# Performance work log

Hardware: AMD Instinct MI355X
Metric: run time of the kernel (lower is better)

Reference implementation:

```python
import jax, jax.numpy as jnp
import numpy as np

E, H, HD = 2048, 32, 64
SCALE = HD ** -0.5


def setup_inputs() -> dict:
    key = jax.random.key(0)
    ks = jax.random.split(key, 11)
    B, T, P = 16, 4, 4096
    S = P + T
    return {
        "hidden_states": jax.random.normal(ks[0], (B, T, E), jnp.float32),
        "past_key": jax.random.normal(ks[1], (1, H, P, HD), jnp.float32),
        "past_value": jax.random.normal(ks[2], (1, H, P, HD), jnp.float32),
        "attention_mask": jnp.zeros((B, 1, T, S), jnp.float32),
        "Wq": jax.random.normal(ks[3], (E, E), jnp.float32) * 0.02,
        "bq": jax.random.normal(ks[4], (E,), jnp.float32) * 0.02,
        "Wk": jax.random.normal(ks[5], (E, E), jnp.float32) * 0.02,
        "bk": jax.random.normal(ks[6], (E,), jnp.float32) * 0.02,
        "Wv": jax.random.normal(ks[7], (E, E), jnp.float32) * 0.02,
        "bv": jax.random.normal(ks[8], (E,), jnp.float32) * 0.02,
        "Wo": jax.random.normal(ks[9], (E, E), jnp.float32) * 0.02,
        "bo": jax.random.normal(ks[10], (E,), jnp.float32) * 0.02,
    }


def _shape(x, B, S):
    # [B,S,E] -> [B,H,S,hd]
    return x.reshape(B, S, H, HD).transpose(0, 2, 1, 3)


def reference(hidden_states, past_key, past_value, attention_mask,
              Wq, bq, Wk, bk, Wv, bv, Wo, bo):
    B, T, _ = hidden_states.shape
    # projections (torch Linear: x @ W.T + b); query pre-scaled
    q = _shape(hidden_states @ Wq.T + bq, B, T) * SCALE   # [B,H,T,hd]
    k_new = _shape(hidden_states @ Wk.T + bk, B, T)       # [B,H,T,hd]
    v_new = _shape(hidden_states @ Wv.T + bv, B, T)
    # cache stored with batch 1, broadcast (torch repeat) to B, then concat
    k_past = jnp.broadcast_to(past_key, (B,) + past_key.shape[1:])
    v_past = jnp.broadcast_to(past_value, (B,) + past_value.shape[1:])
    k = jnp.concatenate([k_past, k_new], axis=2)          # [B,H,S,hd]
    v = jnp.concatenate([v_past, v_new], axis=2)
    scores = jnp.einsum('bhtd,bhsd->bhts', q, k)          # [B,H,T,S]
    scores = scores + attention_mask                      # mask is [B,1,T,S]
    scores = jnp.maximum(scores, jnp.finfo(scores.dtype).min)
    w = jax.nn.softmax(scores, axis=-1)
    out = jnp.einsum('bhts,bhsd->bhtd', w, v)             # [B,H,T,hd]
    out = out.transpose(0, 2, 1, 3).reshape(B, T, E)
    return out @ Wo.T + bo
```

## Files before the change

kernel.cpp:

```cpp
#include <hip/hip_runtime.h>
#include <hip/hip_bf16.h>


typedef float f4 __attribute__((ext_vector_type(4)));
typedef short s8v __attribute__((ext_vector_type(8)));

#define NEG_HUGE (-3.402823466e38f)

__device__ inline unsigned short f2bs(float x) {
  union { float f; unsigned int u; } a; a.f = x;
  unsigned int u = a.u;
  u += 0x7fffu + ((u >> 16) & 1u);
  return (unsigned short)(u >> 16);
}
__device__ inline float bs2f(unsigned short s) {
  union { unsigned int u; float f; } a; a.u = ((unsigned int)s) << 16;
  return a.f;
}
__device__ inline unsigned int pk2(float a, float b) {
  union { __hip_bfloat162 v; unsigned int u; } c;
  c.v = __float22bfloat162_rn(make_float2(a, b));
  return c.u;
}
__device__ inline unsigned long long pack4(float a, float b, float c, float d) {
  return (unsigned long long)pk2(a, b) | ((unsigned long long)pk2(c, d) << 32);
}
__device__ inline s8v cvt8(f4 a, f4 b) {
  union { s8v s; unsigned int u[4]; } r;
  r.u[0] = pk2(a[0], a[1]); r.u[1] = pk2(a[2], a[3]);
  r.u[2] = pk2(b[0], b[1]); r.u[3] = pk2(b[2], b[3]);
  return r.s;
}
__device__ inline f4 mfma16(s8v a, s8v b, f4 c) {
  return __builtin_amdgcn_mfma_f32_16x16x32_bf16(a, b, c, 0, 0, 0);
}
__device__ inline f4 fzero() { f4 z = {0.f,0.f,0.f,0.f}; return z; }
__device__ inline float wave_sum(float v) {
  #pragma unroll
  for (int off = 32; off; off >>= 1) v += __shfl_xor(v, off, 64);
  return v;
}

__global__ __launch_bounds__(256) void k_qkv(
    const float* __restrict__ hs, const float* __restrict__ Wq,
    const float* __restrict__ Wk, const float* __restrict__ Wv,
    float* __restrict__ part) {
  __shared__ __align__(16) unsigned short As[64 * 264];
  const int n0 = blockIdx.x * 64;
  const int k0 = blockIdx.y * 256;
  const int p = n0 >> 11;
  const int c0 = n0 & 2047;
  const float* W = (p == 0) ? Wq : (p == 1) ? Wk : Wv;
  const int t = threadIdx.x, lane = t & 63, w = t >> 6;
  const int cl = lane & 15, quad = lane >> 4;

  #pragma unroll
  for (int i = 0; i < 16; ++i) {
    int idx4 = t + (i << 8);
    int row = idx4 >> 6;
    int col = (idx4 & 63) << 2;
    f4 v = *reinterpret_cast<const f4*>(hs + row * 2048 + k0 + col);
    *reinterpret_cast<unsigned long long*>(&As[row * 264 + col]) =
        pack4(v[0], v[1], v[2], v[3]);
  }
  __syncthreads();

  f4 acc[4];
  #pragma unroll
  for (int i = 0; i < 4; ++i) acc[i] = fzero();

  const int cw = c0 + w * 16 + cl;
  const float* wbase = W + (size_t)cw * 2048 + k0;
  #pragma unroll
  for (int ks2 = 0; ks2 < 8; ++ks2) {
    const int kb = ks2 * 32 + quad * 8;
    f4 w0 = *reinterpret_cast<const f4*>(wbase + kb);
    f4 w1 = *reinterpret_cast<const f4*>(wbase + kb + 4);
    s8v bf = cvt8(w0, w1);
    #pragma unroll
    for (int mt = 0; mt < 4; ++mt) {
      s8v af = *reinterpret_cast<const s8v*>(&As[(mt * 16 + cl) * 264 + kb]);
      acc[mt] = mfma16(af, bf, acc[mt]);
    }
  }
  float* outp = part + (size_t)blockIdx.y * 64 * 6144;
  #pragma unroll
  for (int mt = 0; mt < 4; ++mt)
    #pragma unroll
    for (int rg = 0; rg < 4; ++rg) {
      int r = mt * 16 + quad * 4 + rg;
      outp[r * 6144 + n0 + w * 16 + cl] = acc[mt][rg];
    }
}

__global__ __launch_bounds__(256) void k_qkv_red(
    const float* __restrict__ part, const float* __restrict__ bq,
    const float* __restrict__ bk, const float* __restrict__ bv,
    unsigned short* __restrict__ qws, float* __restrict__ knew,
    float* __restrict__ vnew) {
  const int i4 = blockIdx.x * 256 + threadIdx.x;
  const int base = i4 * 4;
  const int r = base / 6144;
  const int n = base - r * 6144;
  f4 s = *reinterpret_cast<const f4*>(part + base);
  #pragma unroll
  for (int ks = 1; ks < 8; ++ks) {
    f4 p2 = *reinterpret_cast<const f4*>(part + (size_t)ks * 393216 + base);
    #pragma unroll
    for (int j = 0; j < 4; ++j) s[j] += p2[j];
  }
  const int p = n >> 11, c = n & 2047;
  const int h = c >> 6, d = c & 63;
  const int b = r >> 2, tt = r & 3;
  if (p == 0) {
    f4 bb = *reinterpret_cast<const f4*>(bq + c);
    uint2 pw;
    pw.x = pk2((s[0] + bb[0]) * 0.125f, (s[1] + bb[1]) * 0.125f);
    pw.y = pk2((s[2] + bb[2]) * 0.125f, (s[3] + bb[3]) * 0.125f);
    *reinterpret_cast<uint2*>(qws + h * 4608 + r * 72 + d) = pw;
  } else if (p == 1) {
    f4 bb = *reinterpret_cast<const f4*>(bk + c);
    f4 o;
    #pragma unroll
    for (int j = 0; j < 4; ++j) o[j] = s[j] + bb[j];
    *reinterpret_cast<f4*>(knew + ((h * 16 + b) * 4 + tt) * 64 + d) = o;
  } else {
    f4 bb = *reinterpret_cast<const f4*>(bv + c);
    f4 o;
    #pragma unroll
    for (int j = 0; j < 4; ++j) o[j] = s[j] + bb[j];
    *reinterpret_cast<f4*>(vnew + ((h * 16 + b) * 4 + tt) * 64 + d) = o;
  }
}

__global__ __launch_bounds__(256) void k_flash(
    const unsigned short* __restrict__ qws, const float* __restrict__ Kp,
    const float* __restrict__ Vp, const float* __restrict__ mask,
    float* __restrict__ Opart, float* __restrict__ mpart,
    float* __restrict__ lpart) {
  __shared__ __align__(16) unsigned short Pl[64 * 264];
  __shared__ float redm[4 * 64];
  __shared__ float reds[4 * 64];
  const int bx = blockIdx.x;
  const int h = bx & 31, cch = bx >> 5;
  const int s0 = cch * 256;
  const int t = threadIdx.x, lane = t & 63, w = t >> 6;
  const int cl = lane & 15, quad = lane >> 4;
  const float* Kh = Kp + (size_t)h * 4096 * 64;
  const float* Vh = Vp + (size_t)h * 4096 * 64;

  s8v qf[4][2];
  #pragma unroll
  for (int qt = 0; qt < 4; ++qt)
    #pragma unroll
    for (int k2 = 0; k2 < 2; ++k2)
      qf[qt][k2] = *reinterpret_cast<const s8v*>(
          qws + h * 4608 + (qt * 16 + cl) * 72 + k2 * 32 + quad * 8);

  f4 acc[4][4];
  #pragma unroll
  for (int si = 0; si < 4; ++si)
    #pragma unroll
    for (int qt = 0; qt < 4; ++qt)
      acc[si][qt] = *reinterpret_cast<const f4*>(
          mask + (size_t)(qt * 16 + cl) * 4100 + s0 + w * 64 + si * 16 + quad * 4);

  f4 kreg[4][2][2];
  #pragma unroll
  for (int si = 0; si < 4; ++si) {
    const float* kr = Kh + (size_t)(s0 + w * 64 + si * 16 + cl) * 64 + quad * 8;
    #pragma unroll
    for (int k2 = 0; k2 < 2; ++k2) {
      kreg[si][k2][0] = *reinterpret_cast<const f4*>(kr + k2 * 32);
      kreg[si][k2][1] = *reinterpret_cast<const f4*>(kr + k2 * 32 + 4);
    }
  }

  #pragma unroll
  for (int si = 0; si < 4; ++si)
    #pragma unroll
    for (int k2 = 0; k2 < 2; ++k2) {
      s8v ak = cvt8(kreg[si][k2][0], kreg[si][k2][1]);
      #pragma unroll
      for (int qt = 0; qt < 4; ++qt)
        acc[si][qt] = mfma16(ak, qf[qt][k2], acc[si][qt]);
    }

  #pragma unroll
  for (int si = 0; si < 4; ++si)
    #pragma unroll
    for (int qt = 0; qt < 4; ++qt)
      #pragma unroll
      for (int rg = 0; rg < 4; ++rg)
        acc[si][qt][rg] = fmaxf(acc[si][qt][rg], NEG_HUGE);

  #pragma unroll
  for (int qt = 0; qt < 4; ++qt) {
    float m = NEG_HUGE;
    #pragma unroll
    for (int si = 0; si < 4; ++si)
      #pragma unroll
      for (int rg = 0; rg < 4; ++rg) m = fmaxf(m, acc[si][qt][rg]);
    m = fmaxf(m, __shfl_xor(m, 16, 64));
    m = fmaxf(m, __shfl_xor(m, 32, 64));
    if (quad == 0) redm[w * 64 + qt * 16 + cl] = m;
  }
  __syncthreads();

  const int dcol = w * 16 + cl;
  float vr[8][8];
  #pragma unroll
  for (int k2 = 0; k2 < 8; ++k2) {
    const int sb = k2 * 32 + quad * 8;
    const float* vb = Vh + (size_t)(s0 + sb) * 64 + dcol;
    #pragma unroll
    for (int j = 0; j < 8; ++j) vr[k2][j] = vb[j * 64];
  }

  float mq[4];
  #pragma unroll
  for (int qt = 0; qt < 4; ++qt) {
    int q = qt * 16 + cl;
    mq[qt] = fmaxf(fmaxf(redm[q], redm[64 + q]),
                   fmaxf(redm[128 + q], redm[192 + q]));
    if (w == 0 && quad == 0) mpart[(h * 16 + cch) * 64 + q] = mq[qt];
  }
  #pragma unroll
  for (int qt = 0; qt < 4; ++qt) {
    float sum = 0.f;
    #pragma unroll
    for (int si = 0; si < 4; ++si) {
      f4 e;
      #pragma unroll
      for (int rg = 0; rg < 4; ++rg) {
        e[rg] = __expf(acc[si][qt][rg] - mq[qt]);
        sum += e[rg];
      }
      uint2 pw;
      pw.x = pk2(e[0], e[1]);
      pw.y = pk2(e[2], e[3]);
      *reinterpret_cast<uint2*>(
          &Pl[(qt * 16 + cl) * 264 + w * 64 + si * 16 + quad * 4]) = pw;
    }
    sum += __shfl_xor(sum, 16, 64);
    sum += __shfl_xor(sum, 32, 64);
    if (quad == 0) reds[w * 64 + qt * 16 + cl] = sum;
  }
  __syncthreads();

  if (w == 0 && quad == 0) {
    #pragma unroll
    for (int qt = 0; qt < 4; ++qt) {
      int q = qt * 16 + cl;
      lpart[(h * 16 + cch) * 64 + q] =
          reds[q] + reds[64 + q] + reds[128 + q] + reds[192 + q];
    }
  }

  f4 oacc[4];
  #pragma unroll
  for (int mt = 0; mt < 4; ++mt) oacc[mt] = fzero();
  #pragma unroll
  for (int k2 = 0; k2 < 8; ++k2) {
    const int sb = k2 * 32 + quad * 8;
    f4 v0, v1;
    v0[0] = vr[k2][0]; v0[1] = vr[k2][1]; v0[2] = vr[k2][2]; v0[3] = vr[k2][3];
    v1[0] = vr[k2][4]; v1[1] = vr[k2][5]; v1[2] = vr[k2][6]; v1[3] = vr[k2][7];
    s8v bvv = cvt8(v0, v1);
    #pragma unroll
    for (int mt = 0; mt < 4; ++mt) {
      s8v pa = *reinterpret_cast<const s8v*>(&Pl[(mt * 16 + cl) * 264 + sb]);
      oacc[mt] = mfma16(pa, bvv, oacc[mt]);
    }
  }
  float* ob = Opart + (size_t)(h * 16 + cch) * 64 * 64;
  #pragma unroll
  for (int mt = 0; mt < 4; ++mt)
    #pragma unroll
    for (int rg = 0; rg < 4; ++rg)
      ob[(mt * 16 + quad * 4 + rg) * 64 + dcol] = oacc[mt][rg];
}

__global__ __launch_bounds__(256) void k_merge(
    const unsigned short* __restrict__ qws, const float* __restrict__ knew,
    const float* __restrict__ vnew, const float* __restrict__ mask,
    const float* __restrict__ Opart, const float* __restrict__ mpart,
    const float* __restrict__ lpart, unsigned short* __restrict__ attn) {
  const int bx = blockIdx.x;
  const int h = bx & 31, b = bx >> 5;
  const int tt = threadIdx.x >> 6;
  const int d = threadIdx.x & 63;
  const int r = b * 4 + tt;
  float qd = bs2f(qws[h * 4608 + r * 72 + d]);
  float scn[4];
  #pragma unroll
  for (int tp = 0; tp < 4; ++tp) {
    float kn = knew[((h * 16 + b) * 4 + tp) * 64 + d];
    float s = wave_sum(qd * kn);
    s += mask[(size_t)r * 4100 + 4096 + tp];
    scn[tp] = fmaxf(s, NEG_HUGE);
  }
  float mi[16], li[16];
  float mtot = NEG_HUGE;
  #pragma unroll
  for (int i = 0; i < 16; ++i) {
    mi[i] = mpart[(h * 16 + i) * 64 + r];
    li[i] = lpart[(h * 16 + i) * 64 + r];
    mtot = fmaxf(mtot, mi[i]);
  }
  #pragma unroll
  for (int tp = 0; tp < 4; ++tp) mtot = fmaxf(mtot, scn[tp]);
  float ltot = 0.f, od = 0.f;
  #pragma unroll
  for (int i = 0; i < 16; ++i) {
    float fct = __expf(mi[i] - mtot);
    ltot += li[i] * fct;
    od += Opart[((size_t)(h * 16 + i) * 64 + r) * 64 + d] * fct;
  }
  #pragma unroll
  for (int tp = 0; tp < 4; ++tp) {
    float e = __expf(scn[tp] - mtot);
    ltot += e;
    od += e * vnew[((h * 16 + b) * 4 + tp) * 64 + d];
  }
  attn[(size_t)r * 2048 + h * 64 + d] = f2bs(od / ltot);
}

__global__ __launch_bounds__(256) void k_out(
    const unsigned short* __restrict__ attn, const float* __restrict__ Wo,
    float* __restrict__ part) {
  __shared__ __align__(16) unsigned short As[64 * 264];
  const int n0 = blockIdx.x * 64;
  const int ksb = blockIdx.y;
  const int k0 = ksb * 256;
  const int t = threadIdx.x, lane = t & 63, w = t >> 6;
  const int cl = lane & 15, quad = lane >> 4;
  #pragma unroll
  for (int i = 0; i < 8; ++i) {
    int idx8 = t + (i << 8);
    int row = idx8 >> 5;
    int col = (idx8 & 31) << 3;
    *reinterpret_cast<uint4*>(&As[row * 264 + col]) =
        *reinterpret_cast<const uint4*>(attn + (size_t)row * 2048 + k0 + col);
  }
  __syncthreads();
  f4 acc[4];
  #pragma unroll
  for (int i = 0; i < 4; ++i) acc[i] = fzero();
  const int cw = n0 + w * 16 + cl;
  const float* wbase = Wo + (size_t)cw * 2048 + k0;
  #pragma unroll
  for (int ks2 = 0; ks2 < 8; ++ks2) {
    const int kb = ks2 * 32 + quad * 8;
    f4 w0 = *reinterpret_cast<const f4*>(wbase + kb);
    f4 w1 = *reinterpret_cast<const f4*>(wbase + kb + 4);
    s8v bf = cvt8(w0, w1);
    #pragma unroll
    for (int mt = 0; mt < 4; ++mt) {
      s8v af = *reinterpret_cast<const s8v*>(&As[(mt * 16 + cl) * 264 + kb]);
      acc[mt] = mfma16(af, bf, acc[mt]);
    }
  }
  float* op = part + (size_t)ksb * 131072;
  #pragma unroll
  for (int mt = 0; mt < 4; ++mt)
    #pragma unroll
    for (int rg = 0; rg < 4; ++rg) {
      int r = mt * 16 + quad * 4 + rg;
      op[r * 2048 + n0 + w * 16 + cl] = acc[mt][rg];
    }
}

__global__ __launch_bounds__(256) void k_out_red(
    const float* __restrict__ part, const float* __restrict__ bo,
    float* __restrict__ out) {
  const int i4 = blockIdx.x * 256 + threadIdx.x;
  f4 s = *reinterpret_cast<const f4*>(part + (size_t)i4 * 4);
  #pragma unroll
  for (int ks = 1; ks < 8; ++ks) {
    f4 p2 = *reinterpret_cast<const f4*>(part + (size_t)ks * 131072 + (size_t)i4 * 4);
    #pragma unroll
    for (int j = 0; j < 4; ++j) s[j] += p2[j];
  }
  f4 bias = *reinterpret_cast<const f4*>(bo + (i4 & 511) * 4);
  f4 o;
  #pragma unroll
  for (int j = 0; j < 4; ++j) o[j] = s[j] + bias[j];
  *reinterpret_cast<f4*>(out + (size_t)i4 * 4) = o;
}

extern "C" void kernel_launch(void* const* d_in, const int* in_sizes, int n_in,
                              void* d_out, int out_size, void* d_ws, size_t ws_size,
                              hipStream_t stream) {
  const float* hs   = (const float*)d_in[0];
  const float* pk   = (const float*)d_in[1];
  const float* pv   = (const float*)d_in[2];
  const float* mask = (const float*)d_in[3];
  const float* Wq   = (const float*)d_in[4];
  const float* bq   = (const float*)d_in[5];
  const float* Wk   = (const float*)d_in[6];
  const float* bk   = (const float*)d_in[7];
  const float* Wv   = (const float*)d_in[8];
  const float* bv   = (const float*)d_in[9];
  const float* Wo   = (const float*)d_in[10];
  const float* bo   = (const float*)d_in[11];

  float* f = (float*)d_ws;
  float* qkv_part = f;
  float* o_part   = qkv_part + 3145728;
  float* Opart    = o_part   + 1048576;
  float* mpart    = Opart    + 2097152;
  float* lpart    = mpart    + 32768;
  float* knew     = lpart    + 32768;
  float* vnew     = knew     + 131072;
  unsigned short* qws  = (unsigned short*)(vnew + 131072);
  unsigned short* attn = qws + 147456;

  k_qkv<<<dim3(96, 8), 256, 0, stream>>>(hs, Wq, Wk, Wv, qkv_part);
  k_qkv_red<<<384, 256, 0, stream>>>(qkv_part, bq, bk, bv, qws, knew, vnew);
  k_flash<<<512, 256, 0, stream>>>(qws, pk, pv, mask, Opart, mpart, lpart);
  k_merge<<<512, 256, 0, stream>>>(qws, knew, vnew, mask, Opart, mpart, lpart, attn);
  k_out<<<dim3(32, 8), 256, 0, stream>>>(attn, Wo, o_part);
  k_out_red<<<128, 256, 0, stream>>>(o_part, bo, (float*)d_out);
}
```

Before: 197.4 us.

## Fuse QKV split-K reduction into flash and merge kernels, drop reduce launch

Removes the separate k_qkv_red kernel. Each flash block now sums the eight split-K partials for its head's Q slice, adds the bias, scales and stores the result as bf16 in shared memory. The merge kernel sums the partials for its own q, k_new and v_new directly. This saves one kernel launch and the intermediate qws/knew/vnew buffers, but the Q reduction is repeated across the 16 chunk blocks per head, and merge reads the partials with scalar loads.

```diff
diff --git a/kernel.cpp b/kernel.cpp
--- a/kernel.cpp
+++ b/kernel.cpp
@@ -93,52 +93,13 @@
     }
 }
 
-__global__ __launch_bounds__(256) void k_qkv_red(
+__global__ __launch_bounds__(256) void k_flash(
     const float* __restrict__ part, const float* __restrict__ bq,
-    const float* __restrict__ bk, const float* __restrict__ bv,
-    unsigned short* __restrict__ qws, float* __restrict__ knew,
-    float* __restrict__ vnew) {
-  const int i4 = blockIdx.x * 256 + threadIdx.x;
-  const int base = i4 * 4;
-  const int r = base / 6144;
-  const int n = base - r * 6144;
-  f4 s = *reinterpret_cast<const f4*>(part + base);
-  #pragma unroll
-  for (int ks = 1; ks < 8; ++ks) {
-    f4 p2 = *reinterpret_cast<const f4*>(part + (size_t)ks * 393216 + base);
-    #pragma unroll
-    for (int j = 0; j < 4; ++j) s[j] += p2[j];
-  }
-  const int p = n >> 11, c = n & 2047;
-  const int h = c >> 6, d = c & 63;
-  const int b = r >> 2, tt = r & 3;
-  if (p == 0) {
-    f4 bb = *reinterpret_cast<const f4*>(bq + c);
-    uint2 pw;
-    pw.x = pk2((s[0] + bb[0]) * 0.125f, (s[1] + bb[1]) * 0.125f);
-    pw.y = pk2((s[2] + bb[2]) * 0.125f, (s[3] + bb[3]) * 0.125f);
-    *reinterpret_cast<uint2*>(qws + h * 4608 + r * 72 + d) = pw;
-  } else if (p == 1) {
-    f4 bb = *reinterpret_cast<const f4*>(bk + c);
-    f4 o;
-    #pragma unroll
-    for (int j = 0; j < 4; ++j) o[j] = s[j] + bb[j];
-    *reinterpret_cast<f4*>(knew + ((h * 16 + b) * 4 + tt) * 64 + d) = o;
-  } else {
-    f4 bb = *reinterpret_cast<const f4*>(bv + c);
-    f4 o;
-    #pragma unroll
-    for (int j = 0; j < 4; ++j) o[j] = s[j] + bb[j];
-    *reinterpret_cast<f4*>(vnew + ((h * 16 + b) * 4 + tt) * 64 + d) = o;
-  }
-}
-
-__global__ __launch_bounds__(256) void k_flash(
-    const unsigned short* __restrict__ qws, const float* __restrict__ Kp,
-    const float* __restrict__ Vp, const float* __restrict__ mask,
-    float* __restrict__ Opart, float* __restrict__ mpart,
-    float* __restrict__ lpart) {
+    const float* __restrict__ Kp, const float* __restrict__ Vp,
+    const float* __restrict__ mask, float* __restrict__ Opart,
+    float* __restrict__ mpart, float* __restrict__ lpart) {
   __shared__ __align__(16) unsigned short Pl[64 * 264];
+  __shared__ __align__(16) unsigned short Qs[64 * 72];
   __shared__ float redm[4 * 64];
   __shared__ float reds[4 * 64];
   const int bx = blockIdx.x;
@@ -149,13 +110,37 @@
   const float* Kh = Kp + (size_t)h * 4096 * 64;
   const float* Vh = Vp + (size_t)h * 4096 * 64;
 
+  {
+    const int hbase = h * 64;
+    #pragma unroll
+    for (int i = 0; i < 4; ++i) {
+      const int u = t + i * 256;
+      const int row = u >> 4;
+      const int c4 = (u & 15) << 2;
+      const int base = row * 6144 + hbase + c4;
+      f4 s = *reinterpret_cast<const f4*>(part + base);
+      #pragma unroll
+      for (int ks = 1; ks < 8; ++ks) {
+        f4 p2 = *reinterpret_cast<const f4*>(part + (size_t)ks * 393216 + base);
+        #pragma unroll
+        for (int j = 0; j < 4; ++j) s[j] += p2[j];
+      }
+      f4 bb = *reinterpret_cast<const f4*>(bq + hbase + c4);
+      uint2 pw;
+      pw.x = pk2((s[0] + bb[0]) * 0.125f, (s[1] + bb[1]) * 0.125f);
+      pw.y = pk2((s[2] + bb[2]) * 0.125f, (s[3] + bb[3]) * 0.125f);
+      *reinterpret_cast<uint2*>(&Qs[row * 72 + c4]) = pw;
+    }
+  }
+  __syncthreads();
+
   s8v qf[4][2];
   #pragma unroll
   for (int qt = 0; qt < 4; ++qt)
     #pragma unroll
     for (int k2 = 0; k2 < 2; ++k2)
       qf[qt][k2] = *reinterpret_cast<const s8v*>(
-          qws + h * 4608 + (qt * 16 + cl) * 72 + k2 * 32 + quad * 8);
+          &Qs[(qt * 16 + cl) * 72 + k2 * 32 + quad * 8]);
 
   f4 acc[4][4];
   #pragma unroll
@@ -282,21 +267,44 @@
 }
 
 __global__ __launch_bounds__(256) void k_merge(
-    const unsigned short* __restrict__ qws, const float* __restrict__ knew,
-    const float* __restrict__ vnew, const float* __restrict__ mask,
-    const float* __restrict__ Opart, const float* __restrict__ mpart,
-    const float* __restrict__ lpart, unsigned short* __restrict__ attn) {
+    const float* __restrict__ part, const float* __restrict__ bq,
+    const float* __restrict__ bk, const float* __restrict__ bv,
+    const float* __restrict__ mask, const float* __restrict__ Opart,
+    const float* __restrict__ mpart, const float* __restrict__ lpart,
+    unsigned short* __restrict__ attn) {
   const int bx = blockIdx.x;
   const int h = bx & 31, b = bx >> 5;
   const int tt = threadIdx.x >> 6;
   const int d = threadIdx.x & 63;
   const int r = b * 4 + tt;
-  float qd = bs2f(qws[h * 4608 + r * 72 + d]);
+  const int hbase = h * 64;
+
+  float qd;
+  {
+    float s = 0.f;
+    #pragma unroll
+    for (int ks = 0; ks < 8; ++ks)
+      s += part[(size_t)ks * 393216 + r * 6144 + hbase + d];
+    qd = (s + bq[hbase + d]) * 0.125f;
+  }
+  float kn[4], vn[4];
+  #pragma unroll
+  for (int tp = 0; tp < 4; ++tp) {
+    const int rr = b * 4 + tp;
+    float sk = 0.f, sv = 0.f;
+    #pragma unroll
+    for (int ks = 0; ks < 8; ++ks) {
+      sk += part[(size_t)ks * 393216 + rr * 6144 + 2048 + hbase + d];
+      sv += part[(size_t)ks * 393216 + rr * 6144 + 4096 + hbase + d];
+    }
+    kn[tp] = sk + bk[hbase + d];
+    vn[tp] = sv + bv[hbase + d];
+  }
+
   float scn[4];
   #pragma unroll
   for (int tp = 0; tp < 4; ++tp) {
-    float kn = knew[((h * 16 + b) * 4 + tp) * 64 + d];
-    float s = wave_sum(qd * kn);
+    float s = wave_sum(qd * kn[tp]);
     s += mask[(size_t)r * 4100 + 4096 + tp];
     scn[tp] = fmaxf(s, NEG_HUGE);
   }
@@ -321,7 +329,7 @@
   for (int tp = 0; tp < 4; ++tp) {
     float e = __expf(scn[tp] - mtot);
     ltot += e;
-    od += e * vnew[((h * 16 + b) * 4 + tp) * 64 + d];
+    od += e * vn[tp];
   }
   attn[(size_t)r * 2048 + h * 64 + d] = f2bs(od / ltot);
 }
@@ -411,15 +419,12 @@
   float* Opart    = o_part   + 1048576;
   float* mpart    = Opart    + 2097152;
   float* lpart    = mpart    + 32768;
-  float* knew     = lpart    + 32768;
-  float* vnew     = knew     + 131072;
-  unsigned short* qws  = (unsigned short*)(vnew + 131072);
-  unsigned short* attn = qws + 147456;
+  unsigned short* attn = (unsigned short*)(lpart + 32768);
 
   k_qkv<<<dim3(96, 8), 256, 0, stream>>>(hs, Wq, Wk, Wv, qkv_part);
-  k_qkv_red<<<384, 256, 0, stream>>>(qkv_part, bq, bk, bv, qws, knew, vnew);
-  k_flash<<<512, 256, 0, stream>>>(qws, pk, pv, mask, Opart, mpart, lpart);
-  k_merge<<<512, 256, 0, stream>>>(qws, knew, vnew, mask, Opart, mpart, lpart, attn);
+  k_flash<<<512, 256, 0, stream>>>(qkv_part, bq, pk, pv, mask, Opart, mpart, lpart);
+  k_merge<<<512, 256, 0, stream>>>(qkv_part, bq, bk, bv, mask, Opart, mpart,
+                                   lpart, attn);
   k_out<<<dim3(32, 8), 256, 0, stream>>>(attn, Wo, o_part);
   k_out_red<<<128, 256, 0, stream>>>(o_part, bo, (float*)d_out);
 }
```

Result: no change. 197.9 us (+0.2%).

## Double flash-decode block to 512 threads, splitting keys and PV reduction across waves

Applied to the files above, without the earlier changes.

The flash kernel now runs 8 waves per block instead of 4. Each wave covers 32 keys for QK^T and softmax. For the PV product, each wave handles one D tile over half of the key range, and writes a separate partial O slab. The merge kernel sums the two halves. This spreads the per-block K/V loading and MFMA work over more waves to raise memory-level parallelism and latency hiding. The cost is a doubled Opart workspace, extra merge reads, and more LDS reduction entries.

```diff
diff --git a/kernel.cpp b/kernel.cpp
--- a/kernel.cpp
+++ b/kernel.cpp
@@ -133,14 +133,14 @@
   }
 }
 
-__global__ __launch_bounds__(256) void k_flash(
+__global__ __launch_bounds__(512) void k_flash(
     const unsigned short* __restrict__ qws, const float* __restrict__ Kp,
     const float* __restrict__ Vp, const float* __restrict__ mask,
     float* __restrict__ Opart, float* __restrict__ mpart,
     float* __restrict__ lpart) {
   __shared__ __align__(16) unsigned short Pl[64 * 264];
-  __shared__ float redm[4 * 64];
-  __shared__ float reds[4 * 64];
+  __shared__ float redm[8 * 64];
+  __shared__ float reds[8 * 64];
   const int bx = blockIdx.x;
   const int h = bx & 31, cch = bx >> 5;
   const int s0 = cch * 256;
@@ -157,18 +157,18 @@
       qf[qt][k2] = *reinterpret_cast<const s8v*>(
           qws + h * 4608 + (qt * 16 + cl) * 72 + k2 * 32 + quad * 8);
 
-  f4 acc[4][4];
-  #pragma unroll
-  for (int si = 0; si < 4; ++si)
+  f4 acc[2][4];
+  #pragma unroll
+  for (int si = 0; si < 2; ++si)
     #pragma unroll
     for (int qt = 0; qt < 4; ++qt)
       acc[si][qt] = *reinterpret_cast<const f4*>(
-          mask + (size_t)(qt * 16 + cl) * 4100 + s0 + w * 64 + si * 16 + quad * 4);
-
-  f4 kreg[4][2][2];
-  #pragma unroll
-  for (int si = 0; si < 4; ++si) {
-    const float* kr = Kh + (size_t)(s0 + w * 64 + si * 16 + cl) * 64 + quad * 8;
+          mask + (size_t)(qt * 16 + cl) * 4100 + s0 + w * 32 + si * 16 + quad * 4);
+
+  f4 kreg[2][2][2];
+  #pragma unroll
+  for (int si = 0; si < 2; ++si) {
+    const float* kr = Kh + (size_t)(s0 + w * 32 + si * 16 + cl) * 64 + quad * 8;
     #pragma unroll
     for (int k2 = 0; k2 < 2; ++k2) {
       kreg[si][k2][0] = *reinterpret_cast<const f4*>(kr + k2 * 32);
@@ -177,7 +177,7 @@
   }
 
   #pragma unroll
-  for (int si = 0; si < 4; ++si)
+  for (int si = 0; si < 2; ++si)
     #pragma unroll
     for (int k2 = 0; k2 < 2; ++k2) {
       s8v ak = cvt8(kreg[si][k2][0], kreg[si][k2][1]);
@@ -187,7 +187,7 @@
     }
 
   #pragma unroll
-  for (int si = 0; si < 4; ++si)
+  for (int si = 0; si < 2; ++si)
     #pragma unroll
     for (int qt = 0; qt < 4; ++qt)
       #pragma unroll
@@ -198,7 +198,7 @@
   for (int qt = 0; qt < 4; ++qt) {
     float m = NEG_HUGE;
     #pragma unroll
-    for (int si = 0; si < 4; ++si)
+    for (int si = 0; si < 2; ++si)
       #pragma unroll
       for (int rg = 0; rg < 4; ++rg) m = fmaxf(m, acc[si][qt][rg]);
     m = fmaxf(m, __shfl_xor(m, 16, 64));
@@ -207,29 +207,32 @@
   }
   __syncthreads();
 
-  const int dcol = w * 16 + cl;
-  float vr[8][8];
-  #pragma unroll
-  for (int k2 = 0; k2 < 8; ++k2) {
-    const int sb = k2 * 32 + quad * 8;
+  const int dtile = w & 3, khalf = w >> 2;
+  const int dcol = dtile * 16 + cl;
+  float vr[4][8];
+  #pragma unroll
+  for (int k2l = 0; k2l < 4; ++k2l) {
+    const int sb = (khalf * 4 + k2l) * 32 + quad * 8;
     const float* vb = Vh + (size_t)(s0 + sb) * 64 + dcol;
     #pragma unroll
-    for (int j = 0; j < 8; ++j) vr[k2][j] = vb[j * 64];
+    for (int j = 0; j < 8; ++j) vr[k2l][j] = vb[j * 64];
   }
 
   float mq[4];
   #pragma unroll
   for (int qt = 0; qt < 4; ++qt) {
     int q = qt * 16 + cl;
-    mq[qt] = fmaxf(fmaxf(redm[q], redm[64 + q]),
-                   fmaxf(redm[128 + q], redm[192 + q]));
-    if (w == 0 && quad == 0) mpart[(h * 16 + cch) * 64 + q] = mq[qt];
+    float m = redm[q];
+    #pragma unroll
+    for (int ww = 1; ww < 8; ++ww) m = fmaxf(m, redm[ww * 64 + q]);
+    mq[qt] = m;
+    if (w == 0 && quad == 0) mpart[(h * 16 + cch) * 64 + q] = m;
   }
   #pragma unroll
   for (int qt = 0; qt < 4; ++qt) {
     float sum = 0.f;
     #pragma unroll
-    for (int si = 0; si < 4; ++si) {
+    for (int si = 0; si < 2; ++si) {
       f4 e;
       #pragma unroll
       for (int rg = 0; rg < 4; ++rg) {
@@ -240,7 +243,7 @@
       pw.x = pk2(e[0], e[1]);
       pw.y = pk2(e[2], e[3]);
       *reinterpret_cast<uint2*>(
-          &Pl[(qt * 16 + cl) * 264 + w * 64 + si * 16 + quad * 4]) = pw;
+          &Pl[(qt * 16 + cl) * 264 + w * 32 + si * 16 + quad * 4]) = pw;
     }
     sum += __shfl_xor(sum, 16, 64);
     sum += __shfl_xor(sum, 32, 64);
@@ -252,8 +255,10 @@
     #pragma unroll
     for (int qt = 0; qt < 4; ++qt) {
       int q = qt * 16 + cl;
-      lpart[(h * 16 + cch) * 64 + q] =
-          reds[q] + reds[64 + q] + reds[128 + q] + reds[192 + q];
+      float s = reds[q];
+      #pragma unroll
+      for (int ww = 1; ww < 8; ++ww) s += reds[ww * 64 + q];
+      lpart[(h * 16 + cch) * 64 + q] = s;
     }
   }
 
@@ -261,11 +266,11 @@
   #pragma unroll
   for (int mt = 0; mt < 4; ++mt) oacc[mt] = fzero();
   #pragma unroll
-  for (int k2 = 0; k2 < 8; ++k2) {
-    const int sb = k2 * 32 + quad * 8;
+  for (int k2l = 0; k2l < 4; ++k2l) {
+    const int sb = (khalf * 4 + k2l) * 32 + quad * 8;
     f4 v0, v1;
-    v0[0] = vr[k2][0]; v0[1] = vr[k2][1]; v0[2] = vr[k2][2]; v0[3] = vr[k2][3];
-    v1[0] = vr[k2][4]; v1[1] = vr[k2][5]; v1[2] = vr[k2][6]; v1[3] = vr[k2][7];
+    v0[0] = vr[k2l][0]; v0[1] = vr[k2l][1]; v0[2] = vr[k2l][2]; v0[3] = vr[k2l][3];
+    v1[0] = vr[k2l][4]; v1[1] = vr[k2l][5]; v1[2] = vr[k2l][6]; v1[3] = vr[k2l][7];
     s8v bvv = cvt8(v0, v1);
     #pragma unroll
     for (int mt = 0; mt < 4; ++mt) {
@@ -273,7 +278,7 @@
       oacc[mt] = mfma16(pa, bvv, oacc[mt]);
     }
   }
-  float* ob = Opart + (size_t)(h * 16 + cch) * 64 * 64;
+  float* ob = Opart + (size_t)((h * 16 + cch) * 2 + khalf) * 64 * 64;
   #pragma unroll
   for (int mt = 0; mt < 4; ++mt)
     #pragma unroll
@@ -315,7 +320,8 @@
   for (int i = 0; i < 16; ++i) {
     float fct = __expf(mi[i] - mtot);
     ltot += li[i] * fct;
-    od += Opart[((size_t)(h * 16 + i) * 64 + r) * 64 + d] * fct;
+    const size_t ob = (size_t)((h * 16 + i) * 2) * 4096 + r * 64 + d;
+    od += (Opart[ob] + Opart[ob + 4096]) * fct;
   }
   #pragma unroll
   for (int tp = 0; tp < 4; ++tp) {
@@ -409,7 +415,7 @@
   float* qkv_part = f;
   float* o_part   = qkv_part + 3145728;
   float* Opart    = o_part   + 1048576;
-  float* mpart    = Opart    + 2097152;
+  float* mpart    = Opart    + 4194304;
   float* lpart    = mpart    + 32768;
   float* knew     = lpart    + 32768;
   float* vnew     = knew     + 131072;
@@ -418,7 +424,7 @@
 
   k_qkv<<<dim3(96, 8), 256, 0, stream>>>(hs, Wq, Wk, Wv, qkv_part);
   k_qkv_red<<<384, 256, 0, stream>>>(qkv_part, bq, bk, bv, qws, knew, vnew);
-  k_flash<<<512, 256, 0, stream>>>(qws, pk, pv, mask, Opart, mpart, lpart);
+  k_flash<<<512, 512, 0, stream>>>(qws, pk, pv, mask, Opart, mpart, lpart);
   k_merge<<<512, 256, 0, stream>>>(qws, knew, vnew, mask, Opart, mpart, lpart, attn);
   k_out<<<dim3(32, 8), 256, 0, stream>>>(attn, Wo, o_part);
   k_out_red<<<128, 256, 0, stream>>>(o_part, bo, (float*)d_out);
```

Result: slower. 202.4 us (+2.5%).
